# Performance work log

Hardware: AMD Instinct MI355X
Metric: run time of the kernel (lower is better)

Reference implementation:

```python
import jax, jax.numpy as jnp
import numpy as np

N_NODES = 100000
N_EDGES = 1600000
D_IN = 128
D_HID = 128
D_OUT = 64
N_LAYERS = 3
BN_EPS = 1e-5


def _mlp_block(h, W1, b1, g, be, W2, b2):
    # PyG MLP([c_in, h, h]): Linear -> BatchNorm -> ReLU -> Linear (plain last)
    h = h @ W1 + b1                      # [N, h]
    mu = jnp.mean(h, axis=0)
    var = jnp.var(h, axis=0)             # biased var, BN training-mode stats
    h = (h - mu) * jax.lax.rsqrt(var + BN_EPS) * g + be
    h = jax.nn.relu(h)
    return h @ W2 + b2


def setup_inputs() -> dict:
    key = jax.random.key(0)
    ks = jax.random.split(key, 16)
    s_in = 1.0 / np.sqrt(D_IN)
    s_h = 1.0 / np.sqrt(D_HID)
    x = jax.random.normal(ks[0], (N_NODES, D_IN), dtype=jnp.float32)
    edge_index = jax.random.randint(ks[1], (2, N_EDGES), 0, N_NODES, dtype=jnp.int64)
    return {
        "x": x,
        "edge_index": edge_index,
        # stacked per-conv MLP params (all layers are 128->128->128)
        "W1": jax.random.normal(ks[2], (N_LAYERS, D_IN, D_HID), jnp.float32) * s_in,
        "b1": jnp.zeros((N_LAYERS, D_HID), jnp.float32),
        "g1": jnp.ones((N_LAYERS, D_HID), jnp.float32),
        "be1": jnp.zeros((N_LAYERS, D_HID), jnp.float32),
        "W2": jax.random.normal(ks[3], (N_LAYERS, D_HID, D_HID), jnp.float32) * s_h,
        "b2": jnp.zeros((N_LAYERS, D_HID), jnp.float32),
        # final MLP([h, h, out])
        "fW1": jax.random.normal(ks[4], (D_HID, D_HID), jnp.float32) * s_h,
        "fb1": jnp.zeros((D_HID,), jnp.float32),
        "fg1": jnp.ones((D_HID,), jnp.float32),
        "fbe1": jnp.zeros((D_HID,), jnp.float32),
        "fW2": jax.random.normal(ks[5], (D_HID, D_OUT), jnp.float32) * s_h,
        "fb2": jnp.zeros((D_OUT,), jnp.float32),
    }


def reference(x, edge_index, W1, b1, g1, be1, W2, b2, fW1, fb1, fg1, fbe1, fW2, fb2):
    src, dst = edge_index[0], edge_index[1]
    for l in range(N_LAYERS):
        # GINConv, eps=0: nn((1+eps)*x + sum_{j->i} x_j)
        aggr = jax.ops.segment_sum(x[src], dst, num_segments=N_NODES)  # [N, d]
        h = x + aggr
        x = jax.nn.relu(_mlp_block(h, W1[l], b1[l], g1[l], be1[l], W2[l], b2[l]))
    # final MLP (dropout=0.5 is identity in eval mode)
    return _mlp_block(x, fW1, fb1, fg1, fbe1, fW2, fb2)
```

## Files before the change

### kernel.cpp

```cpp
#include <hip/hip_runtime.h>
#include <hip/hip_cooperative_groups.h>

namespace cg = cooperative_groups;

#define NN 100000
#define NE 1600000
#define DD 128
#define CAP 56
#define NGROUP 256
#define NSTRIPE 32

static __device__ __forceinline__ unsigned short f2b(float f) {
  unsigned int x = __float_as_uint(f);
  unsigned int r = x + 0x7fffu + ((x >> 16) & 1u);
  return (unsigned short)(r >> 16);
}
static __device__ __forceinline__ float b2f(unsigned short u) {
  return __uint_as_float(((unsigned int)u) << 16);
}

typedef __attribute__((ext_vector_type(8))) short short8;
typedef __attribute__((ext_vector_type(4))) float f32x4;

union V8 {
  uint4 u4;
  short8 s8;
  unsigned short us[8];
};

__global__ __launch_bounds__(256) void castpack_k(const float* __restrict__ x,
                                                  unsigned short* __restrict__ x16,
                                                  const int* __restrict__ ei,
                                                  int2* __restrict__ packed,
                                                  int* __restrict__ cnt,
                                                  float* __restrict__ stats,
                                                  const float* __restrict__ W1,
                                                  const float* __restrict__ W2,
                                                  const float* __restrict__ fW1,
                                                  const float* __restrict__ fW2,
                                                  unsigned short* __restrict__ wt) {
  __shared__ int modeS;
  const int tid = threadIdx.x;
  if (tid < 64) {
    int v = ei[2 * tid + 1];
    unsigned long long b = __ballot(v != 0);
    if (tid == 0) modeS = (b == 0ull) ? 1 : 0;
  }
  __syncthreads();
  const int mode = modeS;
  const int gid = blockIdx.x * 256 + tid;

  size_t i = (size_t)gid * 8;
  f32x4 a = *(const f32x4*)(x + i);
  f32x4 b = *(const f32x4*)(x + i + 4);
  V8 v;
#pragma unroll
  for (int j = 0; j < 4; ++j) {
    v.us[j] = f2b(a[j]);
    v.us[4 + j] = f2b(b[j]);
  }
  *(uint4*)(x16 + i) = v.u4;

  int s, d;
  if (mode) {
    s = ((const int2*)ei)[gid].x;
    d = ((const int2*)ei)[(size_t)NE + gid].x;
  } else {
    s = ei[gid];
    d = ei[NE + gid];
  }
  packed[gid] = make_int2(s, d);
  if (gid < NN) cnt[gid] = 0;
  if (gid < 4 * NSTRIPE * 256) stats[gid] = 0.f;

  if (blockIdx.x < 480) {
    int bb = blockIdx.x;
    const float* src;
    int moff, N;
    if (bb < 192) {
      int m = bb >> 6;
      src = W1 + m * 16384;
      moff = m * 16384;
      N = 128;
      bb &= 63;
    } else if (bb < 384) {
      int m = (bb - 192) >> 6;
      src = W2 + m * 16384;
      moff = (3 + m) * 16384;
      N = 128;
      bb = (bb - 192) & 63;
    } else if (bb < 448) {
      src = fW1;
      moff = 6 * 16384;
      N = 128;
      bb -= 384;
    } else {
      src = fW2;
      moff = 7 * 16384;
      N = 64;
      bb -= 448;
    }
    int idx = bb * 256 + tid;
    int n = idx >> 7, k = idx & 127;
    if (n < N) wt[moff + idx] = f2b(src[(size_t)k * N + n]);
  }
}

__global__ __launch_bounds__(256) void scatter_k(const int2* __restrict__ packed,
                                                 int* __restrict__ cnt,
                                                 int* __restrict__ csr) {
  const int r = blockIdx.x & 7;
  const int g = blockIdx.x >> 3;
  const int lo = r * (NN / 8), hi = lo + (NN / 8);
  for (int e = g * 256 + threadIdx.x; e < NE; e += NGROUP * 256) {
    int2 sd = packed[e];
    if (sd.y >= lo && sd.y < hi) {
      int c = atomicAdd(&cnt[sd.y], 1);
      if (c < CAP) csr[(size_t)sd.y * CAP + c] = sd.x;
    }
  }
}

__global__ __launch_bounds__(256) void gather_k(const int* __restrict__ cnt,
                                                const int* __restrict__ csr,
                                                const unsigned short* __restrict__ x16,
                                                unsigned short* __restrict__ h16) {
  const int node = blockIdx.x * 16 + (threadIdx.x >> 4);
  const int l = threadIdx.x & 15;
  const int beg = node * CAP;
  const int end = beg + cnt[node];
  V8 v;
  v.u4 = *(const uint4*)(x16 + (size_t)node * DD + l * 8);
  float ac0[8], ac1[8];
#pragma unroll
  for (int j = 0; j < 8; ++j) {
    ac0[j] = b2f(v.us[j]);
    ac1[j] = 0.f;
  }
  int p = beg;
  for (; p + 8 <= end; p += 8) {
    const int s0 = csr[p], s1 = csr[p + 1], s2 = csr[p + 2], s3 = csr[p + 3];
    const int s4 = csr[p + 4], s5 = csr[p + 5], s6 = csr[p + 6], s7 = csr[p + 7];
    V8 w0, w1, w2, w3, w4, w5, w6, w7;
    w0.u4 = *(const uint4*)(x16 + (size_t)s0 * DD + l * 8);
    w1.u4 = *(const uint4*)(x16 + (size_t)s1 * DD + l * 8);
    w2.u4 = *(const uint4*)(x16 + (size_t)s2 * DD + l * 8);
    w3.u4 = *(const uint4*)(x16 + (size_t)s3 * DD + l * 8);
    w4.u4 = *(const uint4*)(x16 + (size_t)s4 * DD + l * 8);
    w5.u4 = *(const uint4*)(x16 + (size_t)s5 * DD + l * 8);
    w6.u4 = *(const uint4*)(x16 + (size_t)s6 * DD + l * 8);
    w7.u4 = *(const uint4*)(x16 + (size_t)s7 * DD + l * 8);
#pragma unroll
    for (int j = 0; j < 8; ++j) {
      ac0[j] += (b2f(w0.us[j]) + b2f(w2.us[j])) + (b2f(w4.us[j]) + b2f(w6.us[j]));
      ac1[j] += (b2f(w1.us[j]) + b2f(w3.us[j])) + (b2f(w5.us[j]) + b2f(w7.us[j]));
    }
  }
  for (; p + 2 <= end; p += 2) {
    const int s0 = csr[p], s1 = csr[p + 1];
    V8 w0, w1;
    w0.u4 = *(const uint4*)(x16 + (size_t)s0 * DD + l * 8);
    w1.u4 = *(const uint4*)(x16 + (size_t)s1 * DD + l * 8);
#pragma unroll
    for (int j = 0; j < 8; ++j) {
      ac0[j] += b2f(w0.us[j]);
      ac1[j] += b2f(w1.us[j]);
    }
  }
  if (p < end) {
    const int s0 = csr[p];
    V8 w0;
    w0.u4 = *(const uint4*)(x16 + (size_t)s0 * DD + l * 8);
#pragma unroll
    for (int j = 0; j < 8; ++j) ac0[j] += b2f(w0.us[j]);
  }
  V8 o;
#pragma unroll
  for (int j = 0; j < 8; ++j) o.us[j] = f2b(ac0[j] + ac1[j]);
  *(uint4*)(h16 + (size_t)node * DD + l * 8) = o.u4;
}

template <int SECONDCOLS, int SECEPI>
__global__ __launch_bounds__(512) void layer_k(const unsigned short* __restrict__ Aptr,
                                               const unsigned short* __restrict__ wT1,
                                               const float* __restrict__ bias1,
                                               const unsigned short* __restrict__ wT2,
                                               const float* __restrict__ bias2,
                                               const float* __restrict__ gamma,
                                               const float* __restrict__ beta,
                                               unsigned short* __restrict__ t16,
                                               void* __restrict__ Cptr,
                                               float* __restrict__ stats,
                                               int ntiles) {
  __shared__ unsigned short bT[128][136];
  __shared__ float scS[128];
  __shared__ float shS[128];
  __shared__ float sS[128];
  __shared__ float s2S[128];
  const int tid = threadIdx.x;
  const int wv = tid >> 6;
  const int lane = tid & 63;
  const int l16 = lane & 15;
  const int quad = lane >> 4;

  for (int i = tid; i < 128 * 16; i += 512) {
    int n = i >> 4, k8 = (i & 15) << 3;
    *(uint4*)&bT[n][k8] = *(const uint4*)(wT1 + n * 128 + k8);
  }
  if (tid < 128) {
    sS[tid] = 0.f;
    s2S[tid] = 0.f;
  }
  __syncthreads();

  for (int m = blockIdx.x; m < ntiles; m += gridDim.x) {
    const int arow = m * 128 + wv * 16 + l16;
    const bool rv = arow < NN;
    V8 afr[4];
#pragma unroll
    for (int kc = 0; kc < 4; ++kc) {
      if (rv) {
        afr[kc].u4 = *(const uint4*)(Aptr + (size_t)arow * DD + kc * 32 + quad * 8);
      } else {
        afr[kc].u4 = make_uint4(0u, 0u, 0u, 0u);
      }
    }
    f32x4 acc[8];
#pragma unroll
    for (int nt = 0; nt < 8; ++nt) acc[nt] = (f32x4)(0.0f);
#pragma unroll
    for (int kc = 0; kc < 4; ++kc) {
      const int k0 = kc * 32 + quad * 8;
#pragma unroll
      for (int nt = 0; nt < 8; ++nt) {
        V8 bf;
        bf.u4 = *(const uint4*)&bT[nt * 16 + l16][k0];
        acc[nt] = __builtin_amdgcn_mfma_f32_16x16x32_bf16(afr[kc].s8, bf.s8, acc[nt], 0, 0, 0);
      }
    }
    const int r0 = m * 128 + wv * 16 + quad * 4;
#pragma unroll
    for (int nt = 0; nt < 8; ++nt) {
      const int col = nt * 16 + l16;
      const float bv = bias1[col];
      float s = 0.f, s2 = 0.f;
#pragma unroll
      for (int i = 0; i < 4; ++i) {
        const int r = r0 + i;
        if (r < NN) {
          unsigned short us = f2b(acc[nt][i] + bv);
          t16[(size_t)r * 128 + col] = us;
          float vr = b2f(us);
          s += vr;
          s2 += vr * vr;
        }
      }
      s += __shfl_xor(s, 16);
      s += __shfl_xor(s, 32);
      s2 += __shfl_xor(s2, 16);
      s2 += __shfl_xor(s2, 32);
      if (quad == 0) {
        atomicAdd(&sS[col], s);
        atomicAdd(&s2S[col], s2);
      }
    }
  }
  __syncthreads();
  if (tid < 128) {
    const int xs = (blockIdx.x & (NSTRIPE - 1)) * 256;
    atomicAdd(&stats[xs + tid], sS[tid]);
    atomicAdd(&stats[xs + 128 + tid], s2S[tid]);
  }

  cg::this_grid().sync();

  for (int i = tid; i < SECONDCOLS * 16; i += 512) {
    int n = i >> 4, k8 = (i & 15) << 3;
    *(uint4*)&bT[n][k8] = *(const uint4*)(wT2 + n * 128 + k8);
  }
  if (tid < 128) {
    float su = 0.f, sq = 0.f;
#pragma unroll
    for (int j = 0; j < NSTRIPE; ++j) {
      su += stats[j * 256 + tid];
      sq += stats[j * 256 + 128 + tid];
    }
    const float inv_n = 1.0f / (float)NN;
    float mu = su * inv_n;
    float var = sq * inv_n - mu * mu;
    float sc = gamma[tid] * rsqrtf(var + 1e-5f);
    scS[tid] = sc;
    shS[tid] = beta[tid] - mu * sc;
  }
  __syncthreads();

  for (int m = blockIdx.x; m < ntiles; m += gridDim.x) {
    const int arow = m * 128 + wv * 16 + l16;
    const bool rv = arow < NN;
    V8 afr[4];
#pragma unroll
    for (int kc = 0; kc < 4; ++kc) {
      if (rv) {
        afr[kc].u4 = *(const uint4*)(t16 + (size_t)arow * 128 + kc * 32 + quad * 8);
      } else {
        afr[kc].u4 = make_uint4(0u, 0u, 0u, 0u);
      }
    }
    f32x4 acc[SECONDCOLS / 16];
#pragma unroll
    for (int nt = 0; nt < SECONDCOLS / 16; ++nt) acc[nt] = (f32x4)(0.0f);
#pragma unroll
    for (int kc = 0; kc < 4; ++kc) {
      const int k0 = kc * 32 + quad * 8;
      V8 af = afr[kc];
#pragma unroll
      for (int j = 0; j < 8; ++j) {
        float f = fmaf(b2f(af.us[j]), scS[k0 + j], shS[k0 + j]);
        af.us[j] = f2b(fmaxf(f, 0.0f));
      }
#pragma unroll
      for (int nt = 0; nt < SECONDCOLS / 16; ++nt) {
        V8 bf;
        bf.u4 = *(const uint4*)&bT[nt * 16 + l16][k0];
        acc[nt] = __builtin_amdgcn_mfma_f32_16x16x32_bf16(af.s8, bf.s8, acc[nt], 0, 0, 0);
      }
    }
    const int r0 = m * 128 + wv * 16 + quad * 4;
#pragma unroll
    for (int nt = 0; nt < SECONDCOLS / 16; ++nt) {
      const int col = nt * 16 + l16;
      const float bv = bias2[col];
#pragma unroll
      for (int i = 0; i < 4; ++i) {
        const int r = r0 + i;
        if (r < NN) {
          float v = acc[nt][i] + bv;
          if (SECEPI == 1) {
            ((unsigned short*)Cptr)[(size_t)r * SECONDCOLS + col] = f2b(fmaxf(v, 0.0f));
          } else {
            ((float*)Cptr)[(size_t)r * SECONDCOLS + col] = v;
          }
        }
      }
    }
  }
}

template <int AMODE, int NCOLS, int EPI, int STATS>
__global__ __launch_bounds__(512) void gemm_k(const unsigned short* __restrict__ Aptr,
                                              const unsigned short* __restrict__ wT,
                                              const float* __restrict__ bias,
                                              const float* __restrict__ bn_stats,
                                              const float* __restrict__ gamma,
                                              const float* __restrict__ beta,
                                              void* __restrict__ Cptr,
                                              float* __restrict__ stats_out) {
  __shared__ unsigned short bT[NCOLS][136];
  __shared__ float biasS[NCOLS];
  __shared__ float scS[128];
  __shared__ float shS[128];
  __shared__ float sS[NCOLS];
  __shared__ float s2S[NCOLS];
  const int tid = threadIdx.x;
  const int wv = tid >> 6;
  const int lane = tid & 63;
  const int l16 = lane & 15;
  const int quad = lane >> 4;
  const int arow = blockIdx.x * 128 + wv * 16 + l16;
  const bool rv = arow < NN;

  V8 afr[4];
#pragma unroll
  for (int kc = 0; kc < 4; ++kc) {
    if (rv) {
      afr[kc].u4 = *(const uint4*)(Aptr + (size_t)arow * DD + kc * 32 + quad * 8);
    } else {
      afr[kc].u4 = make_uint4(0u, 0u, 0u, 0u);
    }
  }
  for (int i = tid; i < NCOLS * 16; i += 512) {
    int n = i >> 4, k8 = (i & 15) << 3;
    *(uint4*)&bT[n][k8] = *(const uint4*)(wT + n * 128 + k8);
  }
  if (tid < NCOLS) biasS[tid] = bias[tid];
  if (AMODE == 2 && tid < 128) {
    float su = 0.f, sq = 0.f;
#pragma unroll
    for (int j = 0; j < NSTRIPE; ++j) {
      su += bn_stats[j * 256 + tid];
      sq += bn_stats[j * 256 + 128 + tid];
    }
    const float inv_n = 1.0f / (float)NN;
    float mu = su * inv_n;
    float var = sq * inv_n - mu * mu;
    float sc = gamma[tid] * rsqrtf(var + 1e-5f);
    scS[tid] = sc;
    shS[tid] = beta[tid] - mu * sc;
  }
  if (STATS && tid < NCOLS) {
    sS[tid] = 0.f;
    s2S[tid] = 0.f;
  }
  __syncthreads();

  f32x4 acc[NCOLS / 16];
#pragma unroll
  for (int nt = 0; nt < NCOLS / 16; ++nt) acc[nt] = (f32x4)(0.0f);
#pragma unroll
  for (int kc = 0; kc < 4; ++kc) {
    const int k0 = kc * 32 + quad * 8;
    V8 af = afr[kc];
    if (AMODE == 2) {
#pragma unroll
      for (int j = 0; j < 8; ++j) {
        float f = fmaf(b2f(af.us[j]), scS[k0 + j], shS[k0 + j]);
        af.us[j] = f2b(fmaxf(f, 0.0f));
      }
    }
#pragma unroll
    for (int nt = 0; nt < NCOLS / 16; ++nt) {
      V8 bf;
      bf.u4 = *(const uint4*)&bT[nt * 16 + l16][k0];
      acc[nt] = __builtin_amdgcn_mfma_f32_16x16x32_bf16(af.s8, bf.s8, acc[nt], 0, 0, 0);
    }
  }
  const int r0 = blockIdx.x * 128 + wv * 16 + quad * 4;
#pragma unroll
  for (int nt = 0; nt < NCOLS / 16; ++nt) {
    const int col = nt * 16 + l16;
    const float bv = biasS[col];
    float s = 0.f, s2 = 0.f;
#pragma unroll
    for (int i = 0; i < 4; ++i) {
      const int r = r0 + i;
      if (r < NN) {
        float v = acc[nt][i] + bv;
        if (EPI == 1) v = fmaxf(v, 0.0f);
        if (EPI == 2) {
          ((float*)Cptr)[(size_t)r * NCOLS + col] = v;
        } else {
          unsigned short us = f2b(v);
          ((unsigned short*)Cptr)[(size_t)r * NCOLS + col] = us;
          if (STATS) {
            float vr = b2f(us);
            s += vr;
            s2 += vr * vr;
          }
        }
      }
    }
    if (STATS) {
      s += __shfl_xor(s, 16);
      s += __shfl_xor(s, 32);
      s2 += __shfl_xor(s2, 16);
      s2 += __shfl_xor(s2, 32);
      if (quad == 0) {
        atomicAdd(&sS[col], s);
        atomicAdd(&s2S[col], s2);
      }
    }
  }
  if (STATS) {
    __syncthreads();
    if (tid < NCOLS) {
      const int xs = (blockIdx.x & (NSTRIPE - 1)) * 256;
      atomicAdd(&stats_out[xs + tid], sS[tid]);
      atomicAdd(&stats_out[xs + 128 + tid], s2S[tid]);
    }
  }
}

extern "C" void kernel_launch(void* const* d_in, const int* in_sizes, int n_in,
                              void* d_out, int out_size, void* d_ws, size_t ws_size,
                              hipStream_t stream) {
  const float* x = (const float*)d_in[0];
  const int* ei = (const int*)d_in[1];
  const float* W1 = (const float*)d_in[2];
  const float* b1 = (const float*)d_in[3];
  const float* g1 = (const float*)d_in[4];
  const float* be1 = (const float*)d_in[5];
  const float* W2 = (const float*)d_in[6];
  const float* b2 = (const float*)d_in[7];
  const float* fW1 = (const float*)d_in[8];
  const float* fb1 = (const float*)d_in[9];
  const float* fg1 = (const float*)d_in[10];
  const float* fbe1 = (const float*)d_in[11];
  const float* fW2 = (const float*)d_in[12];
  const float* fb2 = (const float*)d_in[13];

  char* ws = (char*)d_ws;
  unsigned short* x16 = (unsigned short*)ws;
  unsigned short* h16 = (unsigned short*)(ws + (size_t)25600000);
  unsigned short* t16 = (unsigned short*)(ws + (size_t)51200000);
  int2* packed = (int2*)t16;
  int* csr = (int*)(ws + (size_t)76800000);
  int* cnt = (int*)(ws + (size_t)99200000);
  float* stats = (float*)(ws + (size_t)99600000);
  unsigned short* wt = (unsigned short*)(ws + (size_t)99731072);

  const int vecBlocks = (NN * DD) / (256 * 8);
  const int gemmBlocks = (NN + 127) / 128;
  const int filtBlocks = NGROUP * 8;
  const int nodeBlocks = NN / 16;

  int dev = 0, coop = 0;
  hipGetDevice(&dev);
  hipDeviceGetAttribute(&coop, hipDeviceAttributeCooperativeLaunch, dev);
  int occA = 0, occB = 0;
  hipOccupancyMaxActiveBlocksPerMultiprocessor(&occA, layer_k<128, 1>, 512, 0);
  hipOccupancyMaxActiveBlocksPerMultiprocessor(&occB, layer_k<64, 2>, 512, 0);
  int gridA = occA > 0 ? occA * 256 : 0;
  int gridB = occB > 0 ? occB * 256 : 0;
  if (gridA > gemmBlocks) gridA = gemmBlocks;
  if (gridB > gemmBlocks) gridB = gemmBlocks;
  const bool useCoop = (coop != 0) && (gridA > 0) && (gridB > 0);

  castpack_k<<<vecBlocks, 256, 0, stream>>>(x, x16, ei, packed, cnt, stats, W1,
                                            W2, fW1, fW2, wt);
  scatter_k<<<filtBlocks, 256, 0, stream>>>(packed, cnt, csr);

  int ntiles = gemmBlocks;
  for (int l = 0; l < 3; ++l) {
    gather_k<<<nodeBlocks, 256, 0, stream>>>(cnt, csr, x16, h16);
    if (useCoop) {
      const unsigned short* Ap = h16;
      const unsigned short* w1p = wt + (size_t)l * 16384;
      const float* b1p = b1 + l * 128;
      const unsigned short* w2p = wt + (size_t)(3 + l) * 16384;
      const float* b2p = b2 + l * 128;
      const float* gp = g1 + l * 128;
      const float* bep = be1 + l * 128;
      unsigned short* tp = t16;
      void* cp = (void*)x16;
      float* sp = stats + 256 * NSTRIPE * l;
      void* args[] = {&Ap, &w1p, &b1p, &w2p, &b2p, &gp, &bep, &tp, &cp, &sp, &ntiles};
      hipLaunchCooperativeKernel((void*)layer_k<128, 1>, dim3(gridA), dim3(512),
                                 args, 0, stream);
    } else {
      gemm_k<1, 128, 0, 1><<<gemmBlocks, 512, 0, stream>>>(
          h16, wt + (size_t)l * 16384, b1 + l * 128, nullptr, nullptr, nullptr,
          t16, stats + 256 * NSTRIPE * l);
      gemm_k<2, 128, 1, 0><<<gemmBlocks, 512, 0, stream>>>(
          t16, wt + (size_t)(3 + l) * 16384, b2 + l * 128, stats + 256 * NSTRIPE * l,
          g1 + l * 128, be1 + l * 128, x16, nullptr);
    }
  }

  if (useCoop) {
    const unsigned short* Ap = x16;
    const unsigned short* w1p = wt + (size_t)6 * 16384;
    const float* b1p = fb1;
    const unsigned short* w2p = wt + (size_t)7 * 16384;
    const float* b2p = fb2;
    const float* gp = fg1;
    const float* bep = fbe1;
    unsigned short* tp = t16;
    void* cp = d_out;
    float* sp = stats + 256 * NSTRIPE * 3;
    void* args[] = {&Ap, &w1p, &b1p, &w2p, &b2p, &gp, &bep, &tp, &cp, &sp, &ntiles};
    hipLaunchCooperativeKernel((void*)layer_k<64, 2>, dim3(gridB), dim3(512),
                               args, 0, stream);
  } else {
    gemm_k<1, 128, 0, 1><<<gemmBlocks, 512, 0, stream>>>(
        x16, wt + (size_t)6 * 16384, fb1, nullptr, nullptr, nullptr, t16,
        stats + 256 * NSTRIPE * 3);
    gemm_k<2, 64, 2, 0><<<gemmBlocks, 512, 0, stream>>>(
        t16, wt + (size_t)7 * 16384, fb2, stats + 256 * NSTRIPE * 3, fg1, fbe1,
        (float*)d_out, nullptr);
  }
}
```

Baseline: 551.5 us.

## Fuse neighbor gather into cooperative layer GEMM and decode edges in scatter

The separate gather kernel and its h16 intermediate are dropped on the cooperative path. The layer kernel now sums each row's CSR neighbors straight from x16 while building its A fragments, which saves writing and re-reading a 25.6 MB intermediate and one launch per layer. Edge-index decoding also moves from the cast kernel into the scatter kernel, removing the packed edge buffer. The costs are less coalesced 64-byte row segments, degree imbalance across the 16 rows each wave handles, more register pressure, and each scatter range group now re-reading the raw 64-bit edge array.

```diff
diff --git a/kernel.cpp b/kernel.cpp
--- a/kernel.cpp
+++ b/kernel.cpp
@@ -30,8 +30,6 @@
 
 __global__ __launch_bounds__(256) void castpack_k(const float* __restrict__ x,
                                                   unsigned short* __restrict__ x16,
-                                                  const int* __restrict__ ei,
-                                                  int2* __restrict__ packed,
                                                   int* __restrict__ cnt,
                                                   float* __restrict__ stats,
                                                   const float* __restrict__ W1,
@@ -39,15 +37,7 @@
                                                   const float* __restrict__ fW1,
                                                   const float* __restrict__ fW2,
                                                   unsigned short* __restrict__ wt) {
-  __shared__ int modeS;
   const int tid = threadIdx.x;
-  if (tid < 64) {
-    int v = ei[2 * tid + 1];
-    unsigned long long b = __ballot(v != 0);
-    if (tid == 0) modeS = (b == 0ull) ? 1 : 0;
-  }
-  __syncthreads();
-  const int mode = modeS;
   const int gid = blockIdx.x * 256 + tid;
 
   size_t i = (size_t)gid * 8;
@@ -61,15 +51,6 @@
   }
   *(uint4*)(x16 + i) = v.u4;
 
-  int s, d;
-  if (mode) {
-    s = ((const int2*)ei)[gid].x;
-    d = ((const int2*)ei)[(size_t)NE + gid].x;
-  } else {
-    s = ei[gid];
-    d = ei[NE + gid];
-  }
-  packed[gid] = make_int2(s, d);
   if (gid < NN) cnt[gid] = 0;
   if (gid < 4 * NSTRIPE * 256) stats[gid] = 0.f;
 
@@ -106,17 +87,32 @@
   }
 }
 
-__global__ __launch_bounds__(256) void scatter_k(const int2* __restrict__ packed,
+__global__ __launch_bounds__(256) void scatter_k(const int* __restrict__ ei,
                                                  int* __restrict__ cnt,
                                                  int* __restrict__ csr) {
+  __shared__ int modeS;
+  if (threadIdx.x < 64) {
+    int v = ei[2 * threadIdx.x + 1];
+    unsigned long long b = __ballot(v != 0);
+    if (threadIdx.x == 0) modeS = (b == 0ull) ? 1 : 0;
+  }
+  __syncthreads();
+  const int mode = modeS;
   const int r = blockIdx.x & 7;
   const int g = blockIdx.x >> 3;
   const int lo = r * (NN / 8), hi = lo + (NN / 8);
   for (int e = g * 256 + threadIdx.x; e < NE; e += NGROUP * 256) {
-    int2 sd = packed[e];
-    if (sd.y >= lo && sd.y < hi) {
-      int c = atomicAdd(&cnt[sd.y], 1);
-      if (c < CAP) csr[(size_t)sd.y * CAP + c] = sd.x;
+    int s, d;
+    if (mode) {
+      s = ((const int2*)ei)[e].x;
+      d = ((const int2*)ei)[(size_t)NE + e].x;
+    } else {
+      s = ei[e];
+      d = ei[NE + e];
+    }
+    if (d >= lo && d < hi) {
+      int c = atomicAdd(&cnt[d], 1);
+      if (c < CAP) csr[(size_t)d * CAP + c] = s;
     }
   }
 }
@@ -138,24 +134,6 @@
     ac1[j] = 0.f;
   }
   int p = beg;
-  for (; p + 8 <= end; p += 8) {
-    const int s0 = csr[p], s1 = csr[p + 1], s2 = csr[p + 2], s3 = csr[p + 3];
-    const int s4 = csr[p + 4], s5 = csr[p + 5], s6 = csr[p + 6], s7 = csr[p + 7];
-    V8 w0, w1, w2, w3, w4, w5, w6, w7;
-    w0.u4 = *(const uint4*)(x16 + (size_t)s0 * DD + l * 8);
-    w1.u4 = *(const uint4*)(x16 + (size_t)s1 * DD + l * 8);
-    w2.u4 = *(const uint4*)(x16 + (size_t)s2 * DD + l * 8);
-    w3.u4 = *(const uint4*)(x16 + (size_t)s3 * DD + l * 8);
-    w4.u4 = *(const uint4*)(x16 + (size_t)s4 * DD + l * 8);
-    w5.u4 = *(const uint4*)(x16 + (size_t)s5 * DD + l * 8);
-    w6.u4 = *(const uint4*)(x16 + (size_t)s6 * DD + l * 8);
-    w7.u4 = *(const uint4*)(x16 + (size_t)s7 * DD + l * 8);
-#pragma unroll
-    for (int j = 0; j < 8; ++j) {
-      ac0[j] += (b2f(w0.us[j]) + b2f(w2.us[j])) + (b2f(w4.us[j]) + b2f(w6.us[j]));
-      ac1[j] += (b2f(w1.us[j]) + b2f(w3.us[j])) + (b2f(w5.us[j]) + b2f(w7.us[j]));
-    }
-  }
   for (; p + 2 <= end; p += 2) {
     const int s0 = csr[p], s1 = csr[p + 1];
     V8 w0, w1;
@@ -180,8 +158,10 @@
   *(uint4*)(h16 + (size_t)node * DD + l * 8) = o.u4;
 }
 
-template <int SECONDCOLS, int SECEPI>
+template <int SECONDCOLS, int SECEPI, int GATHER>
 __global__ __launch_bounds__(512) void layer_k(const unsigned short* __restrict__ Aptr,
+                                               const int* __restrict__ cnt,
+                                               const int* __restrict__ csr,
                                                const unsigned short* __restrict__ wT1,
                                                const float* __restrict__ bias1,
                                                const unsigned short* __restrict__ wT2,
@@ -217,12 +197,64 @@
     const int arow = m * 128 + wv * 16 + l16;
     const bool rv = arow < NN;
     V8 afr[4];
-#pragma unroll
-    for (int kc = 0; kc < 4; ++kc) {
+    if (GATHER) {
+      float ac[4][8];
+#pragma unroll
+      for (int kc = 0; kc < 4; ++kc)
+#pragma unroll
+        for (int j = 0; j < 8; ++j) ac[kc][j] = 0.f;
       if (rv) {
-        afr[kc].u4 = *(const uint4*)(Aptr + (size_t)arow * DD + kc * 32 + quad * 8);
-      } else {
-        afr[kc].u4 = make_uint4(0u, 0u, 0u, 0u);
+        const unsigned short* rowp = Aptr + (size_t)arow * DD + quad * 8;
+#pragma unroll
+        for (int kc = 0; kc < 4; ++kc) {
+          V8 vv;
+          vv.u4 = *(const uint4*)(rowp + kc * 32);
+#pragma unroll
+          for (int j = 0; j < 8; ++j) ac[kc][j] = b2f(vv.us[j]);
+        }
+        const int beg = arow * CAP;
+        const int end = beg + cnt[arow];
+        int p = beg;
+        for (; p + 2 <= end; p += 2) {
+          const int s0 = csr[p], s1 = csr[p + 1];
+          const unsigned short* r0 = Aptr + (size_t)s0 * DD + quad * 8;
+          const unsigned short* r1 = Aptr + (size_t)s1 * DD + quad * 8;
+          V8 w0[4], w1[4];
+#pragma unroll
+          for (int kc = 0; kc < 4; ++kc) {
+            w0[kc].u4 = *(const uint4*)(r0 + kc * 32);
+            w1[kc].u4 = *(const uint4*)(r1 + kc * 32);
+          }
+#pragma unroll
+          for (int kc = 0; kc < 4; ++kc)
+#pragma unroll
+            for (int j = 0; j < 8; ++j)
+              ac[kc][j] += b2f(w0[kc].us[j]) + b2f(w1[kc].us[j]);
+        }
+        if (p < end) {
+          const int s0 = csr[p];
+          const unsigned short* r0 = Aptr + (size_t)s0 * DD + quad * 8;
+#pragma unroll
+          for (int kc = 0; kc < 4; ++kc) {
+            V8 w0;
+            w0.u4 = *(const uint4*)(r0 + kc * 32);
+#pragma unroll
+            for (int j = 0; j < 8; ++j) ac[kc][j] += b2f(w0.us[j]);
+          }
+        }
+      }
+#pragma unroll
+      for (int kc = 0; kc < 4; ++kc)
+#pragma unroll
+        for (int j = 0; j < 8; ++j) afr[kc].us[j] = f2b(ac[kc][j]);
+    } else {
+#pragma unroll
+      for (int kc = 0; kc < 4; ++kc) {
+        if (rv) {
+          afr[kc].u4 = *(const uint4*)(Aptr + (size_t)arow * DD + kc * 32 + quad * 8);
+        } else {
+          afr[kc].u4 = make_uint4(0u, 0u, 0u, 0u);
+        }
       }
     }
     f32x4 acc[8];
@@ -492,7 +524,6 @@
   unsigned short* x16 = (unsigned short*)ws;
   unsigned short* h16 = (unsigned short*)(ws + (size_t)25600000);
   unsigned short* t16 = (unsigned short*)(ws + (size_t)51200000);
-  int2* packed = (int2*)t16;
   int* csr = (int*)(ws + (size_t)76800000);
   int* cnt = (int*)(ws + (size_t)99200000);
   float* stats = (float*)(ws + (size_t)99600000);
@@ -507,23 +538,24 @@
   hipGetDevice(&dev);
   hipDeviceGetAttribute(&coop, hipDeviceAttributeCooperativeLaunch, dev);
   int occA = 0, occB = 0;
-  hipOccupancyMaxActiveBlocksPerMultiprocessor(&occA, layer_k<128, 1>, 512, 0);
-  hipOccupancyMaxActiveBlocksPerMultiprocessor(&occB, layer_k<64, 2>, 512, 0);
+  hipOccupancyMaxActiveBlocksPerMultiprocessor(&occA, layer_k<128, 1, 1>, 512, 0);
+  hipOccupancyMaxActiveBlocksPerMultiprocessor(&occB, layer_k<64, 2, 0>, 512, 0);
   int gridA = occA > 0 ? occA * 256 : 0;
   int gridB = occB > 0 ? occB * 256 : 0;
   if (gridA > gemmBlocks) gridA = gemmBlocks;
   if (gridB > gemmBlocks) gridB = gemmBlocks;
   const bool useCoop = (coop != 0) && (gridA > 0) && (gridB > 0);
 
-  castpack_k<<<vecBlocks, 256, 0, stream>>>(x, x16, ei, packed, cnt, stats, W1,
-                                            W2, fW1, fW2, wt);
-  scatter_k<<<filtBlocks, 256, 0, stream>>>(packed, cnt, csr);
+  castpack_k<<<vecBlocks, 256, 0, stream>>>(x, x16, cnt, stats, W1, W2, fW1,
+                                            fW2, wt);
+  scatter_k<<<filtBlocks, 256, 0, stream>>>(ei, cnt, csr);
 
   int ntiles = gemmBlocks;
   for (int l = 0; l < 3; ++l) {
-    gather_k<<<nodeBlocks, 256, 0, stream>>>(cnt, csr, x16, h16);
     if (useCoop) {
-      const unsigned short* Ap = h16;
+      const unsigned short* Ap = x16;
+      const int* cp_ = cnt;
+      const int* cs_ = csr;
       const unsigned short* w1p = wt + (size_t)l * 16384;
       const float* b1p = b1 + l * 128;
       const unsigned short* w2p = wt + (size_t)(3 + l) * 16384;
@@ -533,10 +565,12 @@
       unsigned short* tp = t16;
       void* cp = (void*)x16;
       float* sp = stats + 256 * NSTRIPE * l;
-      void* args[] = {&Ap, &w1p, &b1p, &w2p, &b2p, &gp, &bep, &tp, &cp, &sp, &ntiles};
-      hipLaunchCooperativeKernel((void*)layer_k<128, 1>, dim3(gridA), dim3(512),
-                                 args, 0, stream);
+      void* args[] = {&Ap, &cp_, &cs_, &w1p, &b1p, &w2p, &b2p, &gp, &bep,
+                      &tp, &cp, &sp, &ntiles};
+      hipLaunchCooperativeKernel((void*)layer_k<128, 1, 1>, dim3(gridA),
+                                 dim3(512), args, 0, stream);
     } else {
+      gather_k<<<nodeBlocks, 256, 0, stream>>>(cnt, csr, x16, h16);
       gemm_k<1, 128, 0, 1><<<gemmBlocks, 512, 0, stream>>>(
           h16, wt + (size_t)l * 16384, b1 + l * 128, nullptr, nullptr, nullptr,
           t16, stats + 256 * NSTRIPE * l);
@@ -548,6 +582,8 @@
 
   if (useCoop) {
     const unsigned short* Ap = x16;
+    const int* cp_ = nullptr;
+    const int* cs_ = nullptr;
     const unsigned short* w1p = wt + (size_t)6 * 16384;
     const float* b1p = fb1;
     const unsigned short* w2p = wt + (size_t)7 * 16384;
@@ -557,8 +593,9 @@
     unsigned short* tp = t16;
     void* cp = d_out;
     float* sp = stats + 256 * NSTRIPE * 3;
-    void* args[] = {&Ap, &w1p, &b1p, &w2p, &b2p, &gp, &bep, &tp, &cp, &sp, &ntiles};
-    hipLaunchCooperativeKernel((void*)layer_k<64, 2>, dim3(gridB), dim3(512),
+    void* args[] = {&Ap, &cp_, &cs_, &w1p, &b1p, &w2p, &b2p, &gp, &bep,
+                    &tp, &cp, &sp, &ntiles};
+    hipLaunchCooperativeKernel((void*)layer_k<64, 2, 0>, dim3(gridB), dim3(512),
                                args, 0, stream);
   } else {
     gemm_k<1, 128, 0, 1><<<gemmBlocks, 512, 0, stream>>>(
```

Measured after the change: 562.7 us. +2.0%, slower.

## Fuse edge scatter into cast kernel and drop packed edge buffer

Applied to the files above, without the earlier changes.

The separate scatter kernel is merged into the front cast/weight-transpose kernel. The first 2048 blocks read edge indices directly and build the CSR, and the remaining blocks cast x to bf16 and transpose the weights. This removes the intermediate packed int2 edge array write and read, plus one kernel launch. The count array is now zeroed by a memset beforehand. The scatter blocks now read the raw int64/int32 edge array with a strided pattern, which may cost more bandwidth than reading the packed array did.

```diff
diff --git a/kernel.cpp b/kernel.cpp
--- a/kernel.cpp
+++ b/kernel.cpp
@@ -9,6 +9,7 @@
 #define CAP 56
 #define NGROUP 256
 #define NSTRIPE 32
+#define SCATB 2048
 
 static __device__ __forceinline__ unsigned short f2b(float f) {
   unsigned int x = __float_as_uint(f);
@@ -28,28 +29,49 @@
   unsigned short us[8];
 };
 
-__global__ __launch_bounds__(256) void castpack_k(const float* __restrict__ x,
-                                                  unsigned short* __restrict__ x16,
-                                                  const int* __restrict__ ei,
-                                                  int2* __restrict__ packed,
-                                                  int* __restrict__ cnt,
-                                                  float* __restrict__ stats,
-                                                  const float* __restrict__ W1,
-                                                  const float* __restrict__ W2,
-                                                  const float* __restrict__ fW1,
-                                                  const float* __restrict__ fW2,
-                                                  unsigned short* __restrict__ wt) {
-  __shared__ int modeS;
+__global__ __launch_bounds__(256) void front_k(const int* __restrict__ ei,
+                                               int* __restrict__ cnt,
+                                               int* __restrict__ csr,
+                                               const float* __restrict__ x,
+                                               unsigned short* __restrict__ x16,
+                                               float* __restrict__ stats,
+                                               const float* __restrict__ W1,
+                                               const float* __restrict__ W2,
+                                               const float* __restrict__ fW1,
+                                               const float* __restrict__ fW2,
+                                               unsigned short* __restrict__ wt) {
   const int tid = threadIdx.x;
-  if (tid < 64) {
-    int v = ei[2 * tid + 1];
-    unsigned long long b = __ballot(v != 0);
-    if (tid == 0) modeS = (b == 0ull) ? 1 : 0;
-  }
-  __syncthreads();
-  const int mode = modeS;
-  const int gid = blockIdx.x * 256 + tid;
-
+  if (blockIdx.x < SCATB) {
+    __shared__ int modeS;
+    if (tid < 64) {
+      int v = ei[2 * tid + 1];
+      unsigned long long b = __ballot(v != 0);
+      if (tid == 0) modeS = (b == 0ull) ? 1 : 0;
+    }
+    __syncthreads();
+    const int mode = modeS;
+    const int r = blockIdx.x & 7;
+    const int g = blockIdx.x >> 3;
+    const int lo = r * (NN / 8), hi = lo + (NN / 8);
+    for (int e = g * 256 + tid; e < NE; e += NGROUP * 256) {
+      int s, d;
+      if (mode) {
+        s = ((const int2*)ei)[e].x;
+        d = ((const int2*)ei)[(size_t)NE + e].x;
+      } else {
+        s = ei[e];
+        d = ei[NE + e];
+      }
+      if (d >= lo && d < hi) {
+        int c = atomicAdd(&cnt[d], 1);
+        if (c < CAP) csr[(size_t)d * CAP + c] = s;
+      }
+    }
+    return;
+  }
+
+  const int cb = blockIdx.x - SCATB;
+  const int gid = cb * 256 + tid;
   size_t i = (size_t)gid * 8;
   f32x4 a = *(const f32x4*)(x + i);
   f32x4 b = *(const f32x4*)(x + i + 4);
@@ -61,20 +83,10 @@
   }
   *(uint4*)(x16 + i) = v.u4;
 
-  int s, d;
-  if (mode) {
-    s = ((const int2*)ei)[gid].x;
-    d = ((const int2*)ei)[(size_t)NE + gid].x;
-  } else {
-    s = ei[gid];
-    d = ei[NE + gid];
-  }
-  packed[gid] = make_int2(s, d);
-  if (gid < NN) cnt[gid] = 0;
   if (gid < 4 * NSTRIPE * 256) stats[gid] = 0.f;
 
-  if (blockIdx.x < 480) {
-    int bb = blockIdx.x;
+  if (cb < 480) {
+    int bb = cb;
     const float* src;
     int moff, N;
     if (bb < 192) {
@@ -106,21 +118,6 @@
   }
 }
 
-__global__ __launch_bounds__(256) void scatter_k(const int2* __restrict__ packed,
-                                                 int* __restrict__ cnt,
-                                                 int* __restrict__ csr) {
-  const int r = blockIdx.x & 7;
-  const int g = blockIdx.x >> 3;
-  const int lo = r * (NN / 8), hi = lo + (NN / 8);
-  for (int e = g * 256 + threadIdx.x; e < NE; e += NGROUP * 256) {
-    int2 sd = packed[e];
-    if (sd.y >= lo && sd.y < hi) {
-      int c = atomicAdd(&cnt[sd.y], 1);
-      if (c < CAP) csr[(size_t)sd.y * CAP + c] = sd.x;
-    }
-  }
-}
-
 __global__ __launch_bounds__(256) void gather_k(const int* __restrict__ cnt,
                                                 const int* __restrict__ csr,
                                                 const unsigned short* __restrict__ x16,
@@ -492,7 +489,6 @@
   unsigned short* x16 = (unsigned short*)ws;
   unsigned short* h16 = (unsigned short*)(ws + (size_t)25600000);
   unsigned short* t16 = (unsigned short*)(ws + (size_t)51200000);
-  int2* packed = (int2*)t16;
   int* csr = (int*)(ws + (size_t)76800000);
   int* cnt = (int*)(ws + (size_t)99200000);
   float* stats = (float*)(ws + (size_t)99600000);
@@ -500,7 +496,6 @@
 
   const int vecBlocks = (NN * DD) / (256 * 8);
   const int gemmBlocks = (NN + 127) / 128;
-  const int filtBlocks = NGROUP * 8;
   const int nodeBlocks = NN / 16;
 
   int dev = 0, coop = 0;
@@ -515,9 +510,9 @@
   if (gridB > gemmBlocks) gridB = gemmBlocks;
   const bool useCoop = (coop != 0) && (gridA > 0) && (gridB > 0);
 
-  castpack_k<<<vecBlocks, 256, 0, stream>>>(x, x16, ei, packed, cnt, stats, W1,
-                                            W2, fW1, fW2, wt);
-  scatter_k<<<filtBlocks, 256, 0, stream>>>(packed, cnt, csr);
+  hipMemsetAsync(cnt, 0, NN * sizeof(int), stream);
+  front_k<<<SCATB + vecBlocks, 256, 0, stream>>>(ei, cnt, csr, x, x16, stats,
+                                                 W1, W2, fW1, fW2, wt);
 
   int ntiles = gemmBlocks;
   for (int l = 0; l < 3; ++l) {
```

Result: no change. 549.5 us (-0.4%).
